# Kernel optimization log

Measured on AMD Instinct MI355X. Metric: run time of the kernel, lower is better.

The kernel has to match this reference:

```python
import jax, jax.numpy as jnp
import numpy as np

B, T, D, H, QK = 4, 2048, 1024, 16, 64
MAX_WAVELENGTH = 10000


def apply_rope(x, positions):
    # x: [B, T, H, d]; positions: [B, T] int
    d = x.shape[-1]
    fraction = 2 * jnp.arange(0, d // 2, dtype=jnp.int32) / d
    timescale = MAX_WAVELENGTH ** fraction  # [d/2]
    sinusoid = positions[..., None] / timescale[None, :]  # [B, T, d/2]
    sinusoid = sinusoid[..., None, :]  # [B, T, 1, d/2]
    sin, cos = jnp.sin(sinusoid), jnp.cos(sinusoid)
    x1, x2 = jnp.split(x, 2, axis=-1)
    return jnp.concatenate([x1 * cos - x2 * sin, x2 * cos + x1 * sin], axis=-1).astype(x.dtype)


def rms_norm(x, scale):
    var = jnp.mean(jnp.square(x), axis=-1, keepdims=True)
    return x * jax.lax.rsqrt(var + 1e-6) * (1 + scale)


def setup_inputs() -> dict:
    key = jax.random.key(0)
    ks = jax.random.split(key, 12)
    s = 0.02
    pos = jnp.broadcast_to(jnp.arange(T, dtype=jnp.int32), (B, T))
    causal = jnp.tril(jnp.ones((T, T), dtype=bool))[None, None]  # [1,1,T,T]
    return {
        "q": jax.random.normal(ks[0], (B, T, D), jnp.float32),
        "kv": jax.random.normal(ks[1], (B, T, D), jnp.float32),
        "mask": jnp.broadcast_to(causal, (B, 1, T, T)),
        "q_positions": pos,
        "kv_positions": pos,
        "Wq": jax.random.normal(ks[2], (D, H * QK), jnp.float32) * s,
        "bq": jnp.zeros((H * QK,), jnp.float32),
        "Wk": jax.random.normal(ks[3], (D, H * QK), jnp.float32) * s,
        "bk": jnp.zeros((H * QK,), jnp.float32),
        "Wv": jax.random.normal(ks[4], (D, H * QK), jnp.float32) * s,
        "bv": jnp.zeros((H * QK,), jnp.float32),
        "q_scale": jnp.zeros((QK,), jnp.float32),
        "k_scale": jnp.zeros((QK,), jnp.float32),
        "head_scale": jnp.zeros((1, H, 1), jnp.float32),
        "Wo": jax.random.normal(ks[5], (H * QK, D), jnp.float32) * s,
        "bo": jnp.zeros((D,), jnp.float32),
    }


def reference(q, kv, mask, q_positions, kv_positions, Wq, bq, Wk, bk, Wv, bv,
              q_scale, k_scale, head_scale, Wo, bo):
    qh = (q @ Wq + bq).reshape(B, T, H, QK)
    kh = (kv @ Wk + bk).reshape(B, T, H, QK)
    vh = (kv @ Wv + bv).reshape(B, T, H, QK)
    # qk layer norm (RMSNorm with (1+scale))
    qh = rms_norm(qh, q_scale)
    kh = rms_norm(kh, k_scale)
    # RoPE
    qh = apply_rope(qh, q_positions)
    kh = apply_rope(kh, kv_positions)
    # attention
    logits = jnp.einsum('bthd,bThd->bhtT', qh, kh) / np.sqrt(QK).astype(q.dtype)
    logits = jnp.where(mask, logits, jnp.finfo(logits.dtype).min)
    weights = jax.nn.softmax(logits, axis=-1)
    weights = jnp.where(mask, weights, 0)
    attn = jnp.einsum('bhtT,bThd->bthd', weights, vh)
    attn = attn * (1 + head_scale)  # [1,H,1] broadcasts over (t,h,d)
    return attn.reshape(B, T, H * QK) @ Wo + bo
```

## Files before the change

kernel.cpp:

```cpp
#include <hip/hip_runtime.h>
#include <math.h>

#define BB 4
#define TT 2048
#define DD 1024
#define HH 16
#define QKD 64
#define MM (BB*TT)
#define NN 1024
#define KK 1024

typedef unsigned short u16;
typedef __attribute__((ext_vector_type(8))) short short8;
typedef __attribute__((ext_vector_type(4))) float float4v;

__device__ __forceinline__ u16 f2bf(float f) {
    union { float f; unsigned u; } v; v.f = f;
    unsigned r = (v.u + 0x7FFFu + ((v.u >> 16) & 1u)) >> 16;
    return (u16)r;
}

typedef __attribute__((address_space(3))) unsigned lds_u32_t;
typedef __attribute__((address_space(1))) const unsigned glb_u32_t;
__device__ __forceinline__ void gl2lds16(const u16* g, u16* l) {
    __builtin_amdgcn_global_load_lds((glb_u32_t*)g, (lds_u32_t*)l, 16, 0, 0);
}

__global__ __launch_bounds__(256) void acast_kernel(
    const float* __restrict__ a, const float* __restrict__ b,
    u16* __restrict__ da, u16* __restrict__ db)
{
    const float* s = blockIdx.y ? b : a;
    u16* d = blockIdx.y ? db : da;
    size_t i = ((size_t)blockIdx.x * 256 + threadIdx.x) * 4;
    float4 v = *(const float4*)&s[i];
    ushort4 o = { f2bf(v.x), f2bf(v.y), f2bf(v.z), f2bf(v.w) };
    *(ushort4*)&d[i] = o;
}

__global__ __launch_bounds__(256) void wt_kernel(
    const float* __restrict__ Wq, const float* __restrict__ Wk,
    const float* __restrict__ Wv, const float* __restrict__ Wo,
    u16* __restrict__ dstbase)
{
    const int z = blockIdx.z;
    const float* src = (z == 0) ? Wq : (z == 1) ? Wk : (z == 2) ? Wv : Wo;
    u16* out = dstbase + (size_t)z * (KK * NN);
    const int bi = blockIdx.y, bj = blockIdx.x;
    __shared__ float tile[64][65];
    const int t = threadIdx.x;
    #pragma unroll
    for (int p = 0; p < 4; p++) {
        int idx = p * 256 + t;
        int r = idx >> 4, c4 = (idx & 15) << 2;
        float4 v = *(const float4*)&src[(size_t)(bi * 64 + r) * NN + bj * 64 + c4];
        tile[r][c4 + 0] = v.x; tile[r][c4 + 1] = v.y;
        tile[r][c4 + 2] = v.z; tile[r][c4 + 3] = v.w;
    }
    __syncthreads();
    #pragma unroll
    for (int p = 0; p < 4; p++) {
        int idx = p * 256 + t;
        int rn = idx >> 4, c4 = (idx & 15) << 2;
        ushort4 o = { f2bf(tile[c4 + 0][rn]), f2bf(tile[c4 + 1][rn]),
                      f2bf(tile[c4 + 2][rn]), f2bf(tile[c4 + 3][rn]) };
        *(ushort4*)&out[(size_t)(bj * 64 + rn) * KK + bi * 64 + c4] = o;
    }
}

__device__ __forceinline__ void gemm_mainloop(
    const u16* __restrict__ A, const u16* __restrict__ Bt,
    int m0, int n0, u16* As, u16* Bs, float4v (&acc)[4][4])
{
    const int tid = threadIdx.x;
    const int wave = tid >> 6, lane = tid & 63;
    const int l15 = lane & 15, lg = lane >> 4;
    const int wm = wave >> 1, wn = wave & 1;

    const int lr = lane >> 3;
    const int lc = lane & 7;

    for (int k0 = 0; k0 < KK; k0 += 64) {
        #pragma unroll
        for (int i = 0; i < 4; i++) {
            int chunk = wave * 4 + i;
            int row = chunk * 8 + lr;
            int gcb = lc ^ (row & 7);
            gl2lds16(A  + (size_t)(m0 + row) * KK + k0 + gcb * 8, As + chunk * 512);
            gl2lds16(Bt + (size_t)(n0 + row) * KK + k0 + gcb * 8, Bs + chunk * 512);
        }
        __syncthreads();

        short8 af[2][4], bf[2][4];
        #pragma unroll
        for (int kc = 0; kc < 2; kc++) {
            #pragma unroll
            for (int x = 0; x < 4; x++) {
                int ra = wm * 64 + x * 16 + l15;
                int sa = (kc * 4 + lg) ^ (ra & 7);
                af[kc][x] = *(const short8*)(As + ra * 64 + sa * 8);
                int rb = wn * 64 + x * 16 + l15;
                int sb = (kc * 4 + lg) ^ (rb & 7);
                bf[kc][x] = *(const short8*)(Bs + rb * 64 + sb * 8);
            }
        }
        #pragma unroll
        for (int mi = 0; mi < 4; mi++)
            #pragma unroll
            for (int nj = 0; nj < 4; nj++) {
                acc[mi][nj] = __builtin_amdgcn_mfma_f32_16x16x32_bf16(af[0][mi], bf[0][nj], acc[mi][nj], 0, 0, 0);
                acc[mi][nj] = __builtin_amdgcn_mfma_f32_16x16x32_bf16(af[1][mi], bf[1][nj], acc[mi][nj], 0, 0, 0);
            }
        __syncthreads();
    }
}

__global__ __launch_bounds__(256) void qkv_gemm(
    const u16* __restrict__ qb, const u16* __restrict__ kvb,
    const u16* __restrict__ Wt,
    const float* __restrict__ bq, const float* __restrict__ bk, const float* __restrict__ bv,
    const int* __restrict__ qpos, const int* __restrict__ kpos,
    const float* __restrict__ q_scale, const float* __restrict__ k_scale,
    u16* __restrict__ qh, u16* __restrict__ kh, u16* __restrict__ vh)
{
    __shared__ u16 As[128 * 64];
    __shared__ u16 Bs[128 * 64];

    const int z = blockIdx.z;
    const u16* A        = (z == 0) ? qb : kvb;
    const u16* B        = Wt + (size_t)z * (KK * NN);
    const float* bias   = (z == 0) ? bq : (z == 1) ? bk : bv;
    const float* scl    = (z == 0) ? q_scale : k_scale;
    const int* pos_arr  = (z == 0) ? qpos : kpos;
    u16* dst            = (z == 0) ? qh : (z == 1) ? kh : vh;

    const int m0 = blockIdx.y * 128, n0 = blockIdx.x * 128;

    float4v acc[4][4];
    #pragma unroll
    for (int i = 0; i < 4; i++)
        #pragma unroll
        for (int j = 0; j < 4; j++) acc[i][j] = (float4v){0.f, 0.f, 0.f, 0.f};

    gemm_mainloop(A, B, m0, n0, As, Bs, acc);

    const int lane = threadIdx.x & 63, wave = threadIdx.x >> 6;
    const int l15 = lane & 15, lg = lane >> 4;
    const int wm = wave >> 1, wn = wave & 1;
    const int mbase = m0 + wm * 64;
    const int nbase = n0 + wn * 64;
    const int h = nbase >> 6;

    float bia[4], sc[4];
    #pragma unroll
    for (int nj = 0; nj < 4; nj++) {
        bia[nj] = bias[nbase - (h << 6) + h * 64 + nj * 16 + l15];
        sc[nj]  = 1.0f + scl[nj * 16 + l15];
    }
    float invts[2];
    #pragma unroll
    for (int p = 0; p < 2; p++)
        invts[p] = powf(10000.0f, -(float)(p * 16 + l15) * (1.0f / 32.0f));

    const float QMUL = 0.125f * 1.44269504088896340736f;

    #pragma unroll
    for (int mi = 0; mi < 4; mi++) {
        #pragma unroll
        for (int r = 0; r < 4; r++) {
            const int m = mbase + mi * 16 + lg * 4 + r;
            const int b = m >> 11, t = m & 2047;
            float v[4];
            #pragma unroll
            for (int nj = 0; nj < 4; nj++) v[nj] = acc[mi][nj][r] + bia[nj];

            if (z < 2) {
                float ss = v[0]*v[0] + v[1]*v[1] + v[2]*v[2] + v[3]*v[3];
                ss += __shfl_xor(ss, 1);
                ss += __shfl_xor(ss, 2);
                ss += __shfl_xor(ss, 4);
                ss += __shfl_xor(ss, 8);
                float rn = rsqrtf(ss * (1.0f / 64.0f) + 1e-6f);
                #pragma unroll
                for (int nj = 0; nj < 4; nj++) v[nj] = v[nj] * rn * sc[nj];

                const float pos = (float)pos_arr[b * TT + t];
                #pragma unroll
                for (int p = 0; p < 2; p++) {
                    float ang = pos * invts[p];
                    float s = sinf(ang), c = cosf(ang);
                    float x1 = v[p], x2 = v[p + 2];
                    v[p]     = x1 * c - x2 * s;
                    v[p + 2] = x2 * c + x1 * s;
                }
                if (z == 0) {
                    #pragma unroll
                    for (int nj = 0; nj < 4; nj++) v[nj] *= QMUL;
                }
            }
            u16* op = dst + ((size_t)((b * HH + h) * TT + t)) * QKD + l15;
            #pragma unroll
            for (int nj = 0; nj < 4; nj++) op[nj * 16] = f2bf(v[nj]);
        }
    }
}

__global__ __launch_bounds__(256) void out_gemm(
    const u16* __restrict__ A, const u16* __restrict__ Bt,
    const float* __restrict__ bo, float* __restrict__ out)
{
    __shared__ u16 As[128 * 64];
    __shared__ u16 Bs[128 * 64];

    const int m0 = blockIdx.y * 128, n0 = blockIdx.x * 128;

    float4v acc[4][4];
    #pragma unroll
    for (int i = 0; i < 4; i++)
        #pragma unroll
        for (int j = 0; j < 4; j++) acc[i][j] = (float4v){0.f, 0.f, 0.f, 0.f};

    gemm_mainloop(A, Bt, m0, n0, As, Bs, acc);

    const int lane = threadIdx.x & 63, wave = threadIdx.x >> 6;
    const int l15 = lane & 15, lg = lane >> 4;
    const int wm = wave >> 1, wn = wave & 1;
    const int mbase = m0 + wm * 64;
    const int nbase = n0 + wn * 64;

    float bov[4];
    #pragma unroll
    for (int nj = 0; nj < 4; nj++) bov[nj] = bo[nbase + nj * 16 + l15];

    #pragma unroll
    for (int mi = 0; mi < 4; mi++)
        #pragma unroll
        for (int r = 0; r < 4; r++) {
            const int m = mbase + mi * 16 + lg * 4 + r;
            float* op = out + (size_t)m * NN + nbase + l15;
            #pragma unroll
            for (int nj = 0; nj < 4; nj++)
                op[nj * 16] = acc[mi][nj][r] + bov[nj];
        }
}

#define LSTR 72

__global__ __launch_bounds__(256) void attn_mfma(
    const u16* __restrict__ qh, const u16* __restrict__ kh,
    const u16* __restrict__ vh, const float* __restrict__ head_scale,
    u16* __restrict__ out)
{
    __shared__ u16 Ks[64 * LSTR];
    __shared__ u16 Vt[64 * LSTR];
    __shared__ u16 Ps[4][16 * LSTR];

    const int b = blockIdx.z, h = blockIdx.y, qt = blockIdx.x;
    const int t0 = qt * 64;
    const int tid  = threadIdx.x;
    const int wave = tid >> 6, lane = tid & 63;
    const int l15 = lane & 15, lg = lane >> 4;

    const size_t bh_off = (size_t)(b * HH + h) * TT * QKD;
    const u16* qbh = qh + bh_off;
    const u16* kbh = kh + bh_off;
    const u16* vbh = vh + bh_off;

    short8 qfrag[2];
    #pragma unroll
    for (int kc = 0; kc < 2; kc++)
        qfrag[kc] = *(const short8*)(qbh + (size_t)(t0 + wave * 16 + l15) * QKD
                                      + kc * 32 + lg * 8);

    float4v o_acc[4];
    #pragma unroll
    for (int nt = 0; nt < 4; nt++) o_acc[nt] = (float4v){0.f, 0.f, 0.f, 0.f};
    float m_run[4] = {-INFINITY, -INFINITY, -INFINITY, -INFINITY};
    float l_run[4] = {0.f, 0.f, 0.f, 0.f};

    for (int j0 = 0; j0 <= t0; j0 += 64) {
        #pragma unroll
        for (int r = 0; r < 2; r++) {
            int idx = r * 256 + tid;
            int row = idx >> 3, cb = (idx & 7) * 8;
            short8 k8 = *(const short8*)(kbh + (size_t)(j0 + row) * QKD + cb);
            *(short8*)&Ks[row * LSTR + cb] = k8;

            int j   = tid & 63;
            int dv0 = (tid >> 6) * 8 + r * 32;
            short8 v8 = *(const short8*)(vbh + (size_t)(j0 + j) * QKD + dv0);
            #pragma unroll
            for (int i = 0; i < 8; i++)
                Vt[(dv0 + i) * LSTR + j] = (u16)v8[i];
        }
        __syncthreads();

        float4v sarr[4];
        #pragma unroll
        for (int nt = 0; nt < 4; nt++) {
            float4v s = (float4v){0.f, 0.f, 0.f, 0.f};
            #pragma unroll
            for (int kc = 0; kc < 2; kc++) {
                short8 bfrag = *(const short8*)&Ks[(nt * 16 + l15) * LSTR + kc * 32 + lg * 8];
                s = __builtin_amdgcn_mfma_f32_16x16x32_bf16(qfrag[kc], bfrag, s, 0, 0, 0);
            }
            sarr[nt] = s;
        }

        const int qbase = t0 + wave * 16 + lg * 4;
        if (j0 == t0) {
            #pragma unroll
            for (int nt = 0; nt < 4; nt++) {
                int jkey = j0 + nt * 16 + l15;
                #pragma unroll
                for (int r = 0; r < 4; r++)
                    if (jkey > qbase + r) sarr[nt][r] = -INFINITY;
            }
        }

        float alpha[4], rowsum[4];
        #pragma unroll
        for (int r = 0; r < 4; r++) {
            float m = fmaxf(fmaxf(sarr[0][r], sarr[1][r]), fmaxf(sarr[2][r], sarr[3][r]));
            m = fmaxf(m, __shfl_xor(m, 1));
            m = fmaxf(m, __shfl_xor(m, 2));
            m = fmaxf(m, __shfl_xor(m, 4));
            m = fmaxf(m, __shfl_xor(m, 8));
            float m_new = fmaxf(m_run[r], m);
            alpha[r] = exp2f(m_run[r] - m_new);
            m_run[r] = m_new;
            rowsum[r] = 0.f;
        }
        u16* pw = Ps[wave];
        #pragma unroll
        for (int nt = 0; nt < 4; nt++) {
            #pragma unroll
            for (int r = 0; r < 4; r++) {
                float p = exp2f(sarr[nt][r] - m_run[r]);
                rowsum[r] += p;
                pw[(lg * 4 + r) * LSTR + nt * 16 + l15] = f2bf(p);
            }
        }
        #pragma unroll
        for (int r = 0; r < 4; r++) {
            float rs = rowsum[r];
            rs += __shfl_xor(rs, 1);
            rs += __shfl_xor(rs, 2);
            rs += __shfl_xor(rs, 4);
            rs += __shfl_xor(rs, 8);
            l_run[r] = l_run[r] * alpha[r] + rs;
        }
        #pragma unroll
        for (int nt = 0; nt < 4; nt++)
            #pragma unroll
            for (int r = 0; r < 4; r++)
                o_acc[nt][r] *= alpha[r];

        short8 pf[2];
        #pragma unroll
        for (int kc = 0; kc < 2; kc++)
            pf[kc] = *(const short8*)&pw[l15 * LSTR + kc * 32 + lg * 8];
        #pragma unroll
        for (int nt = 0; nt < 4; nt++) {
            #pragma unroll
            for (int kc = 0; kc < 2; kc++) {
                short8 vfrag = *(const short8*)&Vt[(nt * 16 + l15) * LSTR + kc * 32 + lg * 8];
                o_acc[nt] = __builtin_amdgcn_mfma_f32_16x16x32_bf16(pf[kc], vfrag, o_acc[nt], 0, 0, 0);
            }
        }
        __syncthreads();
    }

    const float hs = 1.0f + head_scale[h];
    #pragma unroll
    for (int r = 0; r < 4; r++) {
        const int q = t0 + wave * 16 + lg * 4 + r;
        const float f = hs / l_run[r];
        u16* op = out + ((size_t)(b * TT + q) * NN) + h * QKD + l15;
        #pragma unroll
        for (int nt = 0; nt < 4; nt++)
            op[nt * 16] = f2bf(o_acc[nt][r] * f);
    }
}

extern "C" void kernel_launch(void* const* d_in, const int* in_sizes, int n_in,
                              void* d_out, int out_size, void* d_ws, size_t ws_size,
                              hipStream_t stream)
{
    const float* q          = (const float*)d_in[0];
    const float* kv         = (const float*)d_in[1];
    const int*   qpos       = (const int*)d_in[3];
    const int*   kpos       = (const int*)d_in[4];
    const float* Wq         = (const float*)d_in[5];
    const float* bq         = (const float*)d_in[6];
    const float* Wk         = (const float*)d_in[7];
    const float* bk         = (const float*)d_in[8];
    const float* Wv         = (const float*)d_in[9];
    const float* bv         = (const float*)d_in[10];
    const float* q_scale    = (const float*)d_in[11];
    const float* k_scale    = (const float*)d_in[12];
    const float* head_scale = (const float*)d_in[13];
    const float* Wo         = (const float*)d_in[14];
    const float* bo         = (const float*)d_in[15];
    float* out = (float*)d_out;

    char* ws = (char*)d_ws;
    u16* qb     = (u16*)(ws);
    u16* kvb    = (u16*)(ws + (16u << 20));
    u16* Wt     = (u16*)(ws + (32u << 20));
    u16* qh_b   = (u16*)(ws + (40u << 20));
    u16* kh_b   = (u16*)(ws + (56u << 20));
    u16* vh_b   = (u16*)(ws + (72u << 20));
    u16* attn_b = (u16*)(ws + (88u << 20));

    acast_kernel<<<dim3(MM * DD / (256 * 4), 2), 256, 0, stream>>>(q, kv, qb, kvb);
    wt_kernel<<<dim3(16, 16, 4), 256, 0, stream>>>(Wq, Wk, Wv, Wo, Wt);
    qkv_gemm<<<dim3(NN / 128, MM / 128, 3), 256, 0, stream>>>(
        qb, kvb, Wt, bq, bk, bv, qpos, kpos, q_scale, k_scale, qh_b, kh_b, vh_b);
    attn_mfma<<<dim3(TT / 64, HH, BB), 256, 0, stream>>>(qh_b, kh_b, vh_b, head_scale, attn_b);
    out_gemm<<<dim3(NN / 128, MM / 128), 256, 0, stream>>>(attn_b, Wt + (size_t)3 * KK * NN, bo, out);
}
```

Baseline: 527.3 us.

## Pair causal query tiles per block and pre-transpose V in QKV epilogue

```diff
diff --git a/kernel.cpp b/kernel.cpp
--- a/kernel.cpp
+++ b/kernel.cpp
@@ -121,7 +121,7 @@
     const float* __restrict__ bq, const float* __restrict__ bk, const float* __restrict__ bv,
     const int* __restrict__ qpos, const int* __restrict__ kpos,
     const float* __restrict__ q_scale, const float* __restrict__ k_scale,
-    u16* __restrict__ qh, u16* __restrict__ kh, u16* __restrict__ vh)
+    u16* __restrict__ qh, u16* __restrict__ kh, u16* __restrict__ vt)
 {
     __shared__ u16 As[128 * 64];
     __shared__ u16 Bs[128 * 64];
@@ -132,7 +132,6 @@
     const float* bias   = (z == 0) ? bq : (z == 1) ? bk : bv;
     const float* scl    = (z == 0) ? q_scale : k_scale;
     const int* pos_arr  = (z == 0) ? qpos : kpos;
-    u16* dst            = (z == 0) ? qh : (z == 1) ? kh : vh;
 
     const int m0 = blockIdx.y * 128, n0 = blockIdx.x * 128;
 
@@ -154,7 +153,7 @@
     float bia[4], sc[4];
     #pragma unroll
     for (int nj = 0; nj < 4; nj++) {
-        bia[nj] = bias[nbase - (h << 6) + h * 64 + nj * 16 + l15];
+        bia[nj] = bias[h * 64 + nj * 16 + l15];
         sc[nj]  = 1.0f + scl[nj * 16 + l15];
     }
     float invts[2];
@@ -197,10 +196,15 @@
                     #pragma unroll
                     for (int nj = 0; nj < 4; nj++) v[nj] *= QMUL;
                 }
-            }
-            u16* op = dst + ((size_t)((b * HH + h) * TT + t)) * QKD + l15;
-            #pragma unroll
-            for (int nj = 0; nj < 4; nj++) op[nj * 16] = f2bf(v[nj]);
+                u16* op = ((z == 0) ? qh : kh)
+                          + ((size_t)((b * HH + h) * TT + t)) * QKD + l15;
+                #pragma unroll
+                for (int nj = 0; nj < 4; nj++) op[nj * 16] = f2bf(v[nj]);
+            } else {
+                #pragma unroll
+                for (int nj = 0; nj < 4; nj++)
+                    vt[((size_t)(b * HH + h) * QKD + nj * 16 + l15) * TT + t] = f2bf(v[nj]);
+            }
         }
     }
 }
@@ -246,17 +250,17 @@
 
 #define LSTR 72
 
-__global__ __launch_bounds__(256) void attn_mfma(
+__global__ __launch_bounds__(256, 4) void attn_mfma(
     const u16* __restrict__ qh, const u16* __restrict__ kh,
-    const u16* __restrict__ vh, const float* __restrict__ head_scale,
+    const u16* __restrict__ vt, const float* __restrict__ head_scale,
     u16* __restrict__ out)
 {
     __shared__ u16 Ks[64 * LSTR];
-    __shared__ u16 Vt[64 * LSTR];
+    __shared__ u16 Vs[64 * LSTR];
     __shared__ u16 Ps[4][16 * LSTR];
 
-    const int b = blockIdx.z, h = blockIdx.y, qt = blockIdx.x;
-    const int t0 = qt * 64;
+    const int b = blockIdx.z, h = blockIdx.y, pi = blockIdx.x;
+    const int t0L = pi * 64, t0H = (31 - pi) * 64;
     const int tid  = threadIdx.x;
     const int wave = tid >> 6, lane = tid & 63;
     const int l15 = lane & 15, lg = lane >> 4;
@@ -264,37 +268,30 @@
     const size_t bh_off = (size_t)(b * HH + h) * TT * QKD;
     const u16* qbh = qh + bh_off;
     const u16* kbh = kh + bh_off;
-    const u16* vbh = vh + bh_off;
-
-    short8 qfrag[2];
-    #pragma unroll
-    for (int kc = 0; kc < 2; kc++)
-        qfrag[kc] = *(const short8*)(qbh + (size_t)(t0 + wave * 16 + l15) * QKD
-                                      + kc * 32 + lg * 8);
-
-    float4v o_acc[4];
-    #pragma unroll
-    for (int nt = 0; nt < 4; nt++) o_acc[nt] = (float4v){0.f, 0.f, 0.f, 0.f};
-    float m_run[4] = {-INFINITY, -INFINITY, -INFINITY, -INFINITY};
-    float l_run[4] = {0.f, 0.f, 0.f, 0.f};
-
-    for (int j0 = 0; j0 <= t0; j0 += 64) {
-        #pragma unroll
-        for (int r = 0; r < 2; r++) {
-            int idx = r * 256 + tid;
-            int row = idx >> 3, cb = (idx & 7) * 8;
-            short8 k8 = *(const short8*)(kbh + (size_t)(j0 + row) * QKD + cb);
-            *(short8*)&Ks[row * LSTR + cb] = k8;
-
-            int j   = tid & 63;
-            int dv0 = (tid >> 6) * 8 + r * 32;
-            short8 v8 = *(const short8*)(vbh + (size_t)(j0 + j) * QKD + dv0);
-            #pragma unroll
-            for (int i = 0; i < 8; i++)
-                Vt[(dv0 + i) * LSTR + j] = (u16)v8[i];
-        }
-        __syncthreads();
-
+    const u16* vtb = vt + bh_off;
+
+    short8 qfL[2], qfH[2];
+    #pragma unroll
+    for (int kc = 0; kc < 2; kc++) {
+        qfL[kc] = *(const short8*)(qbh + (size_t)(t0L + wave * 16 + l15) * QKD + kc * 32 + lg * 8);
+        qfH[kc] = *(const short8*)(qbh + (size_t)(t0H + wave * 16 + l15) * QKD + kc * 32 + lg * 8);
+    }
+
+    float4v oL[4], oH[4];
+    #pragma unroll
+    for (int nt = 0; nt < 4; nt++) {
+        oL[nt] = (float4v){0.f, 0.f, 0.f, 0.f};
+        oH[nt] = (float4v){0.f, 0.f, 0.f, 0.f};
+    }
+    float mL[4] = {-INFINITY, -INFINITY, -INFINITY, -INFINITY};
+    float mH[4] = {-INFINITY, -INFINITY, -INFINITY, -INFINITY};
+    float lL[4] = {0.f, 0.f, 0.f, 0.f};
+    float lH[4] = {0.f, 0.f, 0.f, 0.f};
+
+    u16* pw = Ps[wave];
+
+    auto process = [&](const short8 (&qf)[2], float4v (&o_acc)[4],
+                       float (&m_run)[4], float (&l_run)[4], int t0, int j0) {
         float4v sarr[4];
         #pragma unroll
         for (int nt = 0; nt < 4; nt++) {
@@ -302,13 +299,13 @@
             #pragma unroll
             for (int kc = 0; kc < 2; kc++) {
                 short8 bfrag = *(const short8*)&Ks[(nt * 16 + l15) * LSTR + kc * 32 + lg * 8];
-                s = __builtin_amdgcn_mfma_f32_16x16x32_bf16(qfrag[kc], bfrag, s, 0, 0, 0);
+                s = __builtin_amdgcn_mfma_f32_16x16x32_bf16(qf[kc], bfrag, s, 0, 0, 0);
             }
             sarr[nt] = s;
         }
 
-        const int qbase = t0 + wave * 16 + lg * 4;
         if (j0 == t0) {
+            const int qbase = t0 + wave * 16 + lg * 4;
             #pragma unroll
             for (int nt = 0; nt < 4; nt++) {
                 int jkey = j0 + nt * 16 + l15;
@@ -331,7 +328,6 @@
             m_run[r] = m_new;
             rowsum[r] = 0.f;
         }
-        u16* pw = Ps[wave];
         #pragma unroll
         for (int nt = 0; nt < 4; nt++) {
             #pragma unroll
@@ -364,22 +360,46 @@
         for (int nt = 0; nt < 4; nt++) {
             #pragma unroll
             for (int kc = 0; kc < 2; kc++) {
-                short8 vfrag = *(const short8*)&Vt[(nt * 16 + l15) * LSTR + kc * 32 + lg * 8];
+                short8 vfrag = *(const short8*)&Vs[(nt * 16 + l15) * LSTR + kc * 32 + lg * 8];
                 o_acc[nt] = __builtin_amdgcn_mfma_f32_16x16x32_bf16(pf[kc], vfrag, o_acc[nt], 0, 0, 0);
             }
         }
+    };
+
+    for (int j0 = 0; j0 <= t0H; j0 += 64) {
+        #pragma unroll
+        for (int r = 0; r < 2; r++) {
+            int idx = r * 256 + tid;
+            int row = idx >> 3, cb = (idx & 7) * 8;
+            *(short8*)&Ks[row * LSTR + cb] =
+                *(const short8*)(kbh + (size_t)(j0 + row) * QKD + cb);
+            *(short8*)&Vs[row * LSTR + cb] =
+                *(const short8*)(vtb + (size_t)row * TT + j0 + cb);
+        }
         __syncthreads();
+
+        process(qfH, oH, mH, lH, t0H, j0);
+        if (j0 <= t0L) process(qfL, oL, mL, lL, t0L, j0);
+        __syncthreads();
     }
 
     const float hs = 1.0f + head_scale[h];
     #pragma unroll
     for (int r = 0; r < 4; r++) {
-        const int q = t0 + wave * 16 + lg * 4 + r;
-        const float f = hs / l_run[r];
-        u16* op = out + ((size_t)(b * TT + q) * NN) + h * QKD + l15;
-        #pragma unroll
-        for (int nt = 0; nt < 4; nt++)
-            op[nt * 16] = f2bf(o_acc[nt][r] * f);
+        {
+            const int q = t0L + wave * 16 + lg * 4 + r;
+            const float f = hs / lL[r];
+            u16* op = out + ((size_t)(b * TT + q) * NN) + h * QKD + l15;
+            #pragma unroll
+            for (int nt = 0; nt < 4; nt++) op[nt * 16] = f2bf(oL[nt][r] * f);
+        }
+        {
+            const int q = t0H + wave * 16 + lg * 4 + r;
+            const float f = hs / lH[r];
+            u16* op = out + ((size_t)(b * TT + q) * NN) + h * QKD + l15;
+            #pragma unroll
+            for (int nt = 0; nt < 4; nt++) op[nt * 16] = f2bf(oH[nt][r] * f);
+        }
     }
 }
 
@@ -410,13 +430,13 @@
     u16* Wt     = (u16*)(ws + (32u << 20));
     u16* qh_b   = (u16*)(ws + (40u << 20));
     u16* kh_b   = (u16*)(ws + (56u << 20));
-    u16* vh_b   = (u16*)(ws + (72u << 20));
+    u16* vt_b   = (u16*)(ws + (72u << 20));
     u16* attn_b = (u16*)(ws + (88u << 20));
 
     acast_kernel<<<dim3(MM * DD / (256 * 4), 2), 256, 0, stream>>>(q, kv, qb, kvb);
     wt_kernel<<<dim3(16, 16, 4), 256, 0, stream>>>(Wq, Wk, Wv, Wo, Wt);
     qkv_gemm<<<dim3(NN / 128, MM / 128, 3), 256, 0, stream>>>(
-        qb, kvb, Wt, bq, bk, bv, qpos, kpos, q_scale, k_scale, qh_b, kh_b, vh_b);
-    attn_mfma<<<dim3(TT / 64, HH, BB), 256, 0, stream>>>(qh_b, kh_b, vh_b, head_scale, attn_b);
+        qb, kvb, Wt, bq, bk, bv, qpos, kpos, q_scale, k_scale, qh_b, kh_b, vt_b);
+    attn_mfma<<<dim3(16, HH, BB), 256, 0, stream>>>(qh_b, kh_b, vt_b, head_scale, attn_b);
     out_gemm<<<dim3(NN / 128, MM / 128), 256, 0, stream>>>(attn_b, Wt + (size_t)3 * KK * NN, bo, out);
 }
```

Result: slower. 737.8 us (+39.9%).
